# Kernel tuning notes

Measured on AMD Instinct MI355X. Metric: run time of the kernel, lower is better.

The kernel has to match this reference:

```python
import jax, jax.numpy as jnp
from jax import lax
import numpy as np

T, K, KEND = 2048, 4, 8
D, H, WD = 100, 256, 300
V, DICT, C = 20000, 700000, 18


def _build_end_indexed(starts, lens, ids, valid):
    # Group gazetteer words by their END position (the step at which the
    # lattice char cell consumes the word memory cell), padded to KEND slots.
    e_ids = np.zeros((T, KEND), np.int32)
    e_start = np.zeros((T, KEND), np.int32)
    e_mask = np.zeros((T, KEND), np.int32)
    cnt = np.zeros(T, np.int64)
    for t in range(T):
        for k in range(K):
            if valid[t, k]:
                e = int(starts[t, k] + lens[t, k] - 1)
                if cnt[e] < KEND:
                    e_ids[e, cnt[e]] = ids[t, k]
                    e_start[e, cnt[e]] = starts[t, k]
                    e_mask[e, cnt[e]] = 1
                    cnt[e] += 1
    return jnp.asarray(e_ids), jnp.asarray(e_start), jnp.asarray(e_mask)


def setup_inputs():
    ks = jax.random.split(jax.random.key(0), 24)
    inputs = jax.random.randint(ks[0], (1, T), 0, V, dtype=jnp.int32)
    rng = np.random.default_rng(0)
    lens = rng.integers(0, 8, size=(T, K))          # word length; valid iff >= 2
    ids = rng.integers(1, DICT, size=(T, K))        # gazetteer word ids
    pos = np.broadcast_to(np.arange(T)[:, None], (T, K))
    # forward direction: word starts at t, ends at t+len-1
    valid_f = (lens >= 2) & (pos + lens - 1 < T)
    fw_ids, fw_start, fw_mask = _build_end_indexed(pos, lens, ids, valid_f)
    # backward direction, expressed in the flipped frame: start' = T-1-(t+len-1)
    starts_b = T - 1 - (pos + lens - 1)
    valid_b = (lens >= 2) & (starts_b >= 0)
    bw_ids, bw_start, bw_mask = _build_end_indexed(starts_b, lens, ids, valid_b)
    s = 0.08
    nrm = lambda k, shape: jax.random.normal(k, shape, jnp.float32) * s
    p = {}
    i = 1
    for pre in ("fw", "bw"):
        p[pre + "_W_ih"] = nrm(ks[i], (D, 3 * H)); i += 1
        p[pre + "_W_hh"] = nrm(ks[i], (H, 3 * H)); i += 1
        p[pre + "_b"] = jnp.zeros((3 * H,), jnp.float32)
        p[pre + "_aW_ih"] = nrm(ks[i], (D, H)); i += 1
        p[pre + "_aW_hh"] = nrm(ks[i], (H, H)); i += 1
        p[pre + "_ab"] = jnp.zeros((H,), jnp.float32)
        p[pre + "_wW_ih"] = nrm(ks[i], (WD, 3 * H)); i += 1
        p[pre + "_wW_hh"] = nrm(ks[i], (H, 3 * H)); i += 1
        p[pre + "_wb"] = jnp.zeros((3 * H,), jnp.float32)
    out = dict(inputs=inputs, fw_ids=fw_ids, fw_start=fw_start, fw_mask=fw_mask,
               bw_ids=bw_ids, bw_start=bw_start, bw_mask=bw_mask, length=T,
               E=nrm(ks[20], (V, D)), word_table=nrm(ks[21], (DICT, WD)),
               W_lin=nrm(ks[22], (2 * H, C)), b_lin=jnp.zeros((C,), jnp.float32))
    out.update(p)
    return out


def _lattice_pass(x, wemb, start, mask, W_ih, W_hh, b, aW_ih, aW_hh, ab, wW_ih, wW_hh, wb):
    # x: [T,D]; wemb: [T,KEND,WD]; start/mask: [T,KEND]
    Tn, Hn = x.shape[0], W_hh.shape[0]

    def step(carry, xs):
        h, c, Hh, Ch = carry                        # Hh/Ch: [T,H] history of char states
        t, xt, we_t, st, m = xs
        mf = m.astype(x.dtype)[:, None]             # [KEND,1]
        hs, cs = Hh[st], Ch[st]                     # char state at each word's start pos
        # WordLSTMCell: c^w = sigmoid(f)*c_start + sigmoid(i)*tanh(g)
        wi, wf, wg = jnp.split(we_t @ wW_ih + hs @ wW_hh + wb, 3, axis=-1)
        cw = jax.nn.sigmoid(wf) * cs + jax.nn.sigmoid(wi) * jnp.tanh(wg)
        # MultiInputLSTMCell char gates
        ii, oo, gg = jnp.split(xt @ W_ih + h @ W_hh + b, 3, axis=-1)
        i_s, o_s, g_t = jax.nn.sigmoid(ii), jax.nn.sigmoid(oo), jnp.tanh(gg)
        # extra input gate per word, then exp-normalization over {i, alphas}
        alpha = jax.nn.sigmoid(xt @ aW_ih + cw @ aW_hh + ab)   # [KEND,H]
        e_i = jnp.exp(i_s)                                      # [H]
        e_a = jnp.exp(alpha) * mf                               # masked slots drop out
        c_merge = (e_i * g_t + (e_a * cw).sum(0)) / (e_i + e_a.sum(0))
        c_plain = (1.0 - i_s) * c + i_s * g_t                   # no-word branch (f = 1-i)
        c_new = jnp.where(jnp.any(m > 0), c_merge, c_plain)
        h_new = o_s * jnp.tanh(c_new)
        return (h_new, c_new, Hh.at[t].set(h_new), Ch.at[t].set(c_new)), h_new

    z = lambda *sh: jnp.zeros(sh, x.dtype)
    init = (z(Hn), z(Hn), z(Tn, Hn), z(Tn, Hn))
    _, hseq = lax.scan(step, init, (jnp.arange(Tn), x, wemb, start, mask))
    return hseq                                      # [T,H]


def reference(inputs, fw_ids, fw_start, fw_mask, bw_ids, bw_start, bw_mask, length, E,
              word_table, W_lin, b_lin,
              fw_W_ih, fw_W_hh, fw_b, fw_aW_ih, fw_aW_hh, fw_ab, fw_wW_ih, fw_wW_hh, fw_wb,
              bw_W_ih, bw_W_hh, bw_b, bw_aW_ih, bw_aW_hh, bw_ab, bw_wW_ih, bw_wW_hh, bw_wb):
    x = E[inputs[0]]                                 # [T,D] char embeddings (batch=1)
    hf = _lattice_pass(x, word_table[fw_ids], fw_start, fw_mask,
                       fw_W_ih, fw_W_hh, fw_b, fw_aW_ih, fw_aW_hh, fw_ab,
                       fw_wW_ih, fw_wW_hh, fw_wb)
    hb = _lattice_pass(x[::-1], word_table[bw_ids], bw_start, bw_mask,
                       bw_W_ih, bw_W_hh, bw_b, bw_aW_ih, bw_aW_hh, bw_ab,
                       bw_wW_ih, bw_wW_hh, bw_wb)[::-1]
    return (jnp.concatenate([hf, hb], axis=-1) @ W_lin + b_lin)[None]  # [1,T,C]
```

## Files before the change

### kernel.cpp

```cpp
#include <hip/hip_runtime.h>
#include <hip/hip_bf16.h>


#define TSEQ 2048
#define KEND 8
#define DEMB 100
#define H    256
#define H3   768
#define WD   300
#define CCLS 18
#define NTH  256

typedef __attribute__((ext_vector_type(8))) short bf16x8;
typedef __attribute__((ext_vector_type(4))) float f32x4;

#define LO_AT  0
#define LO_A1  131072
#define LO_VS  131584
#define LO_UR  133120
#define LO_RC  143872
#define LO_A2  152064
#define LO_AWS 156288
#define LO_MT  160384
#define SMEM_SCAN 160640

__device__ __forceinline__ float sigf(float x) { return 1.0f / (1.0f + expf(-x)); }
__device__ __forceinline__ float bf2f(unsigned u) { return __uint_as_float(u << 16); }
__device__ __forceinline__ unsigned f2bf(float f) {
  union { float f; unsigned u; } x; x.f = f;
  unsigned r = x.u + 0x7fffu + ((x.u >> 16) & 1u);
  return r >> 16;
}

__global__ __launch_bounds__(64) void k_pack(
    const float* __restrict__ W_hh_f, const float* __restrict__ wW_hh_f, const float* __restrict__ aW_hh_f,
    const float* __restrict__ W_hh_b, const float* __restrict__ wW_hh_b, const float* __restrict__ aW_hh_b,
    unsigned short* __restrict__ Wpk)
{
  const int T = blockIdx.x, dir = blockIdx.y;
  const int lane = threadIdx.x;
  const float* Wg = dir ? W_hh_b  : W_hh_f;
  const float* Ww = dir ? wW_hh_b : wW_hh_f;
  const float* Wa = dir ? aW_hh_b : aW_hh_f;
  for (int ks = 0; ks < 8; ++ks) {
    bf16x8 sv;
#pragma unroll
    for (int e = 0; e < 8; ++e) {
      const int k = ks * 32 + (lane >> 4) * 8 + e;
      float f;
      if (T < 96) {
        const int c = T * 16 + (lane & 15);
        f = (c < H3) ? Wg[(size_t)k * H3 + c] : Ww[(size_t)k * H3 + (c - H3)];
      } else {
        const int c = (T - 96) * 16 + (lane & 15);
        f = Wa[(size_t)k * H + c];
      }
      sv[e] = (short)f2bf(f);
    }
    *(bf16x8*)(Wpk + (((size_t)dir * 112 + T) * 8 + ks) * 512 + lane * 8) = sv;
  }
}

__global__ __launch_bounds__(256) void k_embed(
    const int* __restrict__ inputs, const float* __restrict__ E,
    const float* __restrict__ W_ih_f, const float* __restrict__ b_f,
    const float* __restrict__ aW_ih_f, const float* __restrict__ ab_f,
    const float* __restrict__ W_ih_b, const float* __restrict__ b_b,
    const float* __restrict__ aW_ih_b, const float* __restrict__ ab_b,
    __hip_bfloat16* __restrict__ xg, float* __restrict__ xa)
{
  const int t = blockIdx.x, dir = blockIdx.y;
  const int tid = threadIdx.x;
  const float* W_ih = dir ? W_ih_b : W_ih_f;
  const float* bb   = dir ? b_b    : b_f;
  const float* aW   = dir ? aW_ih_b : aW_ih_f;
  const float* ab   = dir ? ab_b   : ab_f;
  const int src = dir ? (TSEQ - 1 - t) : t;

  __shared__ float xr[DEMB];
  if (tid < DEMB) xr[tid] = E[(size_t)inputs[src] * DEMB + tid];
  __syncthreads();

  float a0 = bb[tid], a1 = bb[H + tid], a2 = bb[2 * H + tid], a3 = ab[tid];
  for (int r = 0; r < DEMB; r += 4) {
    const float4 e4 = *reinterpret_cast<const float4*>(&xr[r]);
    const float ev[4] = {e4.x, e4.y, e4.z, e4.w};
#pragma unroll
    for (int kk = 0; kk < 4; ++kk) {
      const float* wp = W_ih + (size_t)(r + kk) * H3 + tid;
      a0 += ev[kk] * wp[0];
      a1 += ev[kk] * wp[H];
      a2 += ev[kk] * wp[2 * H];
      a3 += ev[kk] * aW[(size_t)(r + kk) * H + tid];
    }
  }
  __hip_bfloat16* xgrow = xg + ((size_t)dir * TSEQ + t) * H3;
  xgrow[tid]         = __float2bfloat16(a0);
  xgrow[H + tid]     = __float2bfloat16(a1);
  xgrow[2 * H + tid] = __float2bfloat16(a2);
  xa[((size_t)dir * TSEQ + t) * H + tid] = a3;
}

__global__ __launch_bounds__(256) void k_wordgates(
    const int* __restrict__ fw_ids, const int* __restrict__ fw_mask,
    const int* __restrict__ bw_ids, const int* __restrict__ bw_mask,
    const float* __restrict__ word_table,
    const float* __restrict__ wW_ih_f, const float* __restrict__ wb_f,
    const float* __restrict__ wW_ih_b, const float* __restrict__ wb_b,
    __hip_bfloat16* __restrict__ wg)
{
  const int t = blockIdx.x, dir = blockIdx.y;
  const int tid = threadIdx.x;
  const int* ids = (dir ? bw_ids : fw_ids) + t * KEND;
  const int* msk = (dir ? bw_mask : fw_mask) + t * KEND;
  const float* wW = dir ? wW_ih_b : wW_ih_f;
  const float* wb = dir ? wb_b    : wb_f;

  __shared__ float we[KEND][WD];
  for (int w = 0; w < KEND; ++w) {
    if (msk[w]) {
      const float* src = word_table + (size_t)ids[w] * WD;
      for (int i = tid; i < WD; i += 256) we[w][i] = src[i];
    }
  }
  __syncthreads();

  __hip_bfloat16* out = wg + ((size_t)dir * TSEQ + t) * KEND * H3;
  for (int w = 0; w < KEND; ++w) {
    if (!msk[w]) continue;
    float a0 = wb[tid], a1 = wb[H + tid], a2 = wb[2 * H + tid];
    for (int r = 0; r < WD; r += 4) {
      const float4 e4 = *reinterpret_cast<const float4*>(&we[w][r]);
      const float ev[4] = {e4.x, e4.y, e4.z, e4.w};
#pragma unroll
      for (int kk = 0; kk < 4; ++kk) {
        const float* wp = wW + (size_t)(r + kk) * H3 + tid;
        a0 += ev[kk] * wp[0];
        a1 += ev[kk] * wp[H];
        a2 += ev[kk] * wp[2 * H];
      }
    }
    out[w * H3 + tid]         = __float2bfloat16(a0);
    out[w * H3 + H + tid]     = __float2bfloat16(a1);
    out[w * H3 + 2 * H + tid] = __float2bfloat16(a2);
  }
}

__global__ __launch_bounds__(NTH, 1) void k_scan(
    const __hip_bfloat16* __restrict__ xg, const float* __restrict__ xa,
    const __hip_bfloat16* __restrict__ wgG, float* __restrict__ hseq,
    const int* __restrict__ fw_start, const int* __restrict__ fw_mask,
    const int* __restrict__ bw_start, const int* __restrict__ bw_mask,
    const unsigned short* __restrict__ Wpk,
    unsigned long long* __restrict__ xb, unsigned* __restrict__ xf)
{
  const int gid = blockIdx.x;
  if (gid != 0 && gid != 1 && gid != 8 && gid != 9) return;
  const int dir  = gid & 1;
  const int side = gid >> 3;

  extern __shared__ char smem[];
  unsigned short* A1_16 = (unsigned short*)(smem + LO_A1);
  unsigned short* vS16  = (unsigned short*)(smem + LO_VS);
  unsigned short* ur16  = (unsigned short*)(smem + LO_UR);
  float* ringC = (float*)(smem + LO_RC);
  unsigned short* awS16 = (unsigned short*)(smem + LO_AWS);
  int* metaI = (int*)(smem + LO_MT);

  const int tid  = threadIdx.x;
  const int lane = tid & 63;
  const int wv   = tid >> 6;
  const int lmod = lane & 15;
  const int lgrp = lane >> 4;

  const int* startA = dir ? bw_start : fw_start;
  const int* maskA  = dir ? bw_mask  : fw_mask;
  const char* WpkD = (const char*)(Wpk + (size_t)dir * 112 * 8 * 512);

  unsigned long long* myPay = xb + (size_t)((dir * 2 + side) * 2) * 192;
  const unsigned long long* peerPay = xb + (size_t)((dir * 2 + (side ^ 1)) * 2) * 192;
  unsigned* myFlag   = xf + (dir * 2 + side) * 32;
  unsigned* peerFlag = xf + (dir * 2 + (side ^ 1)) * 32;

  bf16x8 rW[12][8];
  {
    const char* rp = WpkD + (size_t)(side * 48 + wv * 12) * 8192 + lane * 16;
#pragma unroll
    for (int n = 0; n < 12; ++n)
#pragma unroll
      for (int ks = 0; ks < 8; ++ks)
        rW[n][ks] = *(const bf16x8*)(rp + (n * 8 + ks) * 1024);
  }
  for (int o = tid * 16; o < 131072; o += NTH * 16)
    *(uint4*)(smem + LO_AT + o) = *(const uint4*)(WpkD + (size_t)96 * 8192 + o);
  if (tid < 32) *(uint4*)(smem + LO_A1 + tid * 16) = uint4{0, 0, 0, 0};
  for (int o = tid * 16; o < 4224; o += NTH * 16)
    *(uint4*)(smem + LO_A2 + o) = uint4{0, 0, 0, 0};
  for (int o = tid * 16; o < 8192; o += NTH * 16)
    *(uint4*)(smem + LO_RC + o) = uint4{0, 0, 0, 0};

  unsigned nxI = 0, nxO = 0, nxG = 0; float nxA = 0.f;
  unsigned cxI = 0, cxO = 0, cxG = 0; float cxA = 0.f;
  int nmt = 0;
  {
    const unsigned short* xr = (const unsigned short*)(xg + (size_t)dir * TSEQ * H3);
    nxI = xr[tid]; nxO = xr[H + tid]; nxG = xr[2 * H + tid];
    nxA = xa[(size_t)dir * TSEQ * H + tid];
    if (wv == 3) {
      if (lane < 8) nmt = maskA[lane];
      else if (lane < 16) nmt = startA[lane - 8];
    }
  }
  __syncthreads();
  if (wv == 3) {
    int mAll[8], sAll[8];
#pragma unroll
    for (int s = 0; s < 8; ++s) { mAll[s] = __shfl(nmt, s); sAll[s] = __shfl(nmt, 8 + s); }
    if (lane == 0) {
      int n = 0;
      for (int s = 0; s < 8; ++s)
        if (mAll[s]) { metaI[1 + n] = s; metaI[9 + n] = sAll[s]; ++n; }
      metaI[0] = n;
    }
  }
  cxI = nxI; cxO = nxO; cxG = nxG; cxA = nxA;
  __syncthreads();

  for (int t = 0; t < TSEQ; ++t) {
    const int par = t & 1;
    const int* mp = metaI + par * 32;
    const int nw = mp[0];
    const int us7 = (t + 6) % 7;
    unsigned short* stage16 = side ? (ur16 + us7 * 768) : vS16;
    unsigned short* rcv16   = side ? vS16 : (ur16 + us7 * 768);

    unsigned short wgv[24];
#pragma unroll
    for (int it = 0; it < 8; ++it) {
      const int u0 = tid + it * NTH;
      if (u0 < nw * 256) {
        const int w = u0 >> 8, j = u0 & 255;
        const int slot = mp[1 + w];
        const unsigned short* wgp =
            (const unsigned short*)wgG + ((size_t)(dir * TSEQ + t) * KEND + slot) * H3 + j;
        wgv[it * 3 + 0] = wgp[0];
        wgv[it * 3 + 1] = wgp[256];
        wgv[it * 3 + 2] = wgp[512];
      }
    }

#pragma unroll
    for (int g = 0; g < 2; ++g) {
      f32x4 acc[6];
#pragma unroll
      for (int n = 0; n < 6; ++n) acc[n] = f32x4{0.f, 0.f, 0.f, 0.f};
#pragma unroll
      for (int ks = 0; ks < 8; ++ks) {
        const bf16x8 av = *(const bf16x8*)(smem + LO_A1 + ks * 64 + lgrp * 16);
#pragma unroll
        for (int n = 0; n < 6; ++n)
          acc[n] = __builtin_amdgcn_mfma_f32_16x16x32_bf16(av, rW[g * 6 + n][ks], acc[n], 0, 0, 0);
      }
      if (lane < 16) {
#pragma unroll
        for (int n = 0; n < 6; ++n)
          stage16[(wv * 12 + g * 6 + n) * 16 + lane] = (unsigned short)f2bf(acc[n][0]);
      }
    }
    __syncthreads();

    if (tid < 192) {
      const unsigned long long q = *(const unsigned long long*)((const char*)stage16 + tid * 8);
      __hip_atomic_store(myPay + par * 192 + tid, q, __ATOMIC_RELAXED, __HIP_MEMORY_SCOPE_AGENT);
    }
    {
      const int tn = (t + 1 < TSEQ) ? t + 1 : TSEQ - 1;
      const unsigned short* xr = (const unsigned short*)(xg + ((size_t)dir * TSEQ + tn) * H3);
      nxI = xr[tid]; nxO = xr[H + tid]; nxG = xr[2 * H + tid];
      nxA = xa[((size_t)dir * TSEQ + tn) * H + tid];
      if (wv == 3) {
        if (lane < 8) nmt = maskA[tn * KEND + lane];
        else if (lane < 16) nmt = startA[tn * KEND + (lane - 8)];
      }
    }
#pragma unroll
    for (int it = 0; it < 8; ++it) {
      const int u0 = tid + it * NTH;
      if (u0 < nw * 256) {
        const int w = u0 >> 8, j = u0 & 255;
        const int s = mp[9 + w];
        if (side == 1 || s != t - 1) {
          const unsigned short* ur = ur16 + (s % 7) * 768;
          const float wi  = bf2f(wgv[it * 3 + 0]) + bf2f(ur[j]);
          const float wf  = bf2f(wgv[it * 3 + 1]) + bf2f(ur[256 + j]);
          const float wgg = bf2f(wgv[it * 3 + 2]) + bf2f(ur[512 + j]);
          const float cs  = ringC[(s & 7) * 256 + j];
          const float cv  = sigf(wf) * cs + sigf(wi) * tanhf(wgg);
          *(unsigned short*)(smem + LO_A2 + w * 528 + j * 2) = (unsigned short)f2bf(cv);
        }
      }
    }
    __syncthreads();

    if (tid == 0) {
      __hip_atomic_store(myFlag, (unsigned)(t + 1), __ATOMIC_RELAXED, __HIP_MEMORY_SCOPE_AGENT);
      while (__hip_atomic_load(peerFlag, __ATOMIC_RELAXED, __HIP_MEMORY_SCOPE_AGENT) < (unsigned)(t + 1))
        __builtin_amdgcn_s_sleep(1);
    }
    __syncthreads();

    if (tid < 192) {
      const unsigned long long q =
          __hip_atomic_load(peerPay + par * 192 + tid, __ATOMIC_RELAXED, __HIP_MEMORY_SCOPE_AGENT);
      *(unsigned long long*)((char*)rcv16 + tid * 8) = q;
    }
    __syncthreads();

    if (side == 0) {
#pragma unroll
      for (int it = 0; it < 8; ++it) {
        const int u0 = tid + it * NTH;
        if (u0 < nw * 256) {
          const int w = u0 >> 8, j = u0 & 255;
          const int s = mp[9 + w];
          if (s == t - 1) {
            const unsigned short* ur = ur16 + (s % 7) * 768;
            const float wi  = bf2f(wgv[it * 3 + 0]) + bf2f(ur[j]);
            const float wf  = bf2f(wgv[it * 3 + 1]) + bf2f(ur[256 + j]);
            const float wgg = bf2f(wgv[it * 3 + 2]) + bf2f(ur[512 + j]);
            const float cs  = ringC[(s & 7) * 256 + j];
            const float cv  = sigf(wf) * cs + sigf(wi) * tanhf(wgg);
            *(unsigned short*)(smem + LO_A2 + w * 528 + j * 2) = (unsigned short)f2bf(cv);
          }
        }
      }
    }
    __syncthreads();

    if (nw > 0) {
      const int r2 = (lmod > 7) ? 7 : lmod;
      f32x4 ac[4];
#pragma unroll
      for (int m = 0; m < 4; ++m) ac[m] = f32x4{0.f, 0.f, 0.f, 0.f};
#pragma unroll
      for (int ks = 0; ks < 8; ++ks) {
        const bf16x8 a2v = *(const bf16x8*)(smem + LO_A2 + r2 * 528 + ks * 64 + lgrp * 16);
#pragma unroll
        for (int m = 0; m < 4; ++m) {
          const bf16x8 b = *(const bf16x8*)(smem + LO_AT + (size_t)(wv * 4 + m) * 8192 + ks * 1024 + lane * 16);
          ac[m] = __builtin_amdgcn_mfma_f32_16x16x32_bf16(a2v, b, ac[m], 0, 0, 0);
        }
      }
#pragma unroll
      for (int m = 0; m < 4; ++m) {
#pragma unroll
        for (int r = 0; r < 4; ++r) {
          const int row = lgrp * 4 + r;
          if (row < nw) awS16[row * 256 + (wv * 4 + m) * 16 + lmod] = (unsigned short)f2bf(ac[m][r]);
        }
      }
    }
    __syncthreads();

    {
      const int j = tid;
      const float i_s = sigf(bf2f(cxI) + bf2f(vS16[j]));
      const float o_s = sigf(bf2f(cxO) + bf2f(vS16[256 + j]));
      const float g_t = tanhf(bf2f(cxG) + bf2f(vS16[512 + j]));
      float cnew;
      if (nw > 0) {
        const float e_i = expf(i_s);
        float num = e_i * g_t, den = e_i;
        for (int w = 0; w < nw; ++w) {
          const float a  = sigf(cxA + bf2f(awS16[w * 256 + j]));
          const float ea = expf(a);
          num += ea * bf2f(*(const unsigned short*)(smem + LO_A2 + w * 528 + j * 2));
          den += ea;
        }
        cnew = num / den;
      } else {
        cnew = (1.f - i_s) * ringC[((t - 1) & 7) * 256 + j] + i_s * g_t;
      }
      const float hnew = o_s * tanhf(cnew);
      ringC[(t & 7) * 256 + j] = cnew;
      A1_16[j] = (unsigned short)f2bf(hnew);
      if (side == 0) hseq[((size_t)dir * TSEQ + t) * H + j] = hnew;
    }
    if (wv == 3) {
      int mAll[8], sAll[8];
#pragma unroll
      for (int s = 0; s < 8; ++s) { mAll[s] = __shfl(nmt, s); sAll[s] = __shfl(nmt, 8 + s); }
      if (lane == 0) {
        int* mq = metaI + ((t + 1) & 1) * 32;
        int n = 0;
        for (int s = 0; s < 8; ++s)
          if (mAll[s]) { mq[1 + n] = s; mq[9 + n] = sAll[s]; ++n; }
        mq[0] = n;
      }
    }
    cxI = nxI; cxO = nxO; cxG = nxG; cxA = nxA;
    __syncthreads();
  }
}

__global__ __launch_bounds__(64) void k_proj(
    const float* __restrict__ hseq, const float* __restrict__ W_lin,
    const float* __restrict__ b_lin, float* __restrict__ out)
{
  const int t = blockIdx.x;
  const int tid = threadIdx.x;
  __shared__ float hrow[2 * H];
  for (int i = tid; i < H; i += 64) {
    hrow[i]     = hseq[(size_t)t * H + i];
    hrow[H + i] = hseq[((size_t)TSEQ + (TSEQ - 1 - t)) * H + i];
  }
  __syncthreads();
  if (tid < CCLS) {
    float acc = b_lin[tid];
    for (int j = 0; j < 2 * H; ++j) acc += hrow[j] * W_lin[(size_t)j * CCLS + tid];
    out[(size_t)t * CCLS + tid] = acc;
  }
}

extern "C" void kernel_launch(void* const* d_in, const int* in_sizes, int n_in,
                              void* d_out, int out_size, void* d_ws, size_t ws_size,
                              hipStream_t stream)
{
  const int* inputs   = (const int*)d_in[0];
  const int* fw_ids   = (const int*)d_in[1];
  const int* fw_start = (const int*)d_in[2];
  const int* fw_mask  = (const int*)d_in[3];
  const int* bw_ids   = (const int*)d_in[4];
  const int* bw_start = (const int*)d_in[5];
  const int* bw_mask  = (const int*)d_in[6];
  const float* E          = (const float*)d_in[8];
  const float* word_table = (const float*)d_in[9];
  const float* W_lin      = (const float*)d_in[10];
  const float* b_lin      = (const float*)d_in[11];
  const float* fw_W_ih  = (const float*)d_in[12];
  const float* fw_W_hh  = (const float*)d_in[13];
  const float* fw_b     = (const float*)d_in[14];
  const float* fw_aW_ih = (const float*)d_in[15];
  const float* fw_aW_hh = (const float*)d_in[16];
  const float* fw_ab    = (const float*)d_in[17];
  const float* fw_wW_ih = (const float*)d_in[18];
  const float* fw_wW_hh = (const float*)d_in[19];
  const float* fw_wb    = (const float*)d_in[20];
  const float* bw_W_ih  = (const float*)d_in[21];
  const float* bw_W_hh  = (const float*)d_in[22];
  const float* bw_b     = (const float*)d_in[23];
  const float* bw_aW_ih = (const float*)d_in[24];
  const float* bw_aW_hh = (const float*)d_in[25];
  const float* bw_ab    = (const float*)d_in[26];
  const float* bw_wW_ih = (const float*)d_in[27];
  const float* bw_wW_hh = (const float*)d_in[28];
  const float* bw_wb    = (const float*)d_in[29];

  char* p = (char*)d_ws;
  __hip_bfloat16* xg = (__hip_bfloat16*)p;  p += (size_t)2 * TSEQ * H3 * 2;
  float* xa   = (float*)p;                  p += (size_t)2 * TSEQ * H * 4;
  float* hseq = (float*)p;                  p += (size_t)2 * TSEQ * H * 4;
  __hip_bfloat16* wg = (__hip_bfloat16*)p;  p += (size_t)2 * TSEQ * KEND * H3 * 2;
  unsigned short* Wpk = (unsigned short*)p; p += (size_t)2 * 112 * 8 * 512 * 2;
  unsigned long long* xb = (unsigned long long*)p; p += (size_t)2 * 2 * 2 * 192 * 8;
  unsigned* xf = (unsigned*)p;              p += 512;

  hipFuncSetAttribute((const void*)k_scan,
                      hipFuncAttributeMaxDynamicSharedMemorySize, SMEM_SCAN);
  hipMemsetAsync(xf, 0, 512, stream);

  k_pack<<<dim3(112, 2), 64, 0, stream>>>(
      fw_W_hh, fw_wW_hh, fw_aW_hh, bw_W_hh, bw_wW_hh, bw_aW_hh, Wpk);
  k_embed<<<dim3(TSEQ, 2), 256, 0, stream>>>(
      inputs, E, fw_W_ih, fw_b, fw_aW_ih, fw_ab, bw_W_ih, bw_b, bw_aW_ih, bw_ab, xg, xa);
  k_wordgates<<<dim3(TSEQ, 2), 256, 0, stream>>>(
      fw_ids, fw_mask, bw_ids, bw_mask, word_table, fw_wW_ih, fw_wb, bw_wW_ih, bw_wb, wg);
  k_scan<<<16, NTH, SMEM_SCAN, stream>>>(
      xg, xa, wg, hseq, fw_start, fw_mask, bw_start, bw_mask, Wpk, xb, xf);
  k_proj<<<TSEQ, 64, 0, stream>>>(hseq, W_lin, b_lin, (float*)d_out);
}
```

Baseline: 14.37 ms.

## Overlap word-cell attention MFMA with peer handshake and skip redundant passes

Signal the step flag right after publishing the payload, then compute the attention-gate MFMA for words whose cell does not depend on the previous step while waiting for the peer block. A second MFMA pass and its barriers run only when some word starts at t-1. The spin-wait drops its sleep, and the hseq write is split between the two sides. This aims to hide cross-block sync latency and remove barriers from steps without late words. The cost is a duplicated MFMA pass on steps that have such words and a busier spin loop.

After: 16.80 ms. +16.9%, slower.

```diff
diff --git a/kernel.cpp b/kernel.cpp
--- a/kernel.cpp
+++ b/kernel.cpp
@@ -233,6 +233,8 @@
     const int us7 = (t + 6) % 7;
     unsigned short* stage16 = side ? (ur16 + us7 * 768) : vS16;
     unsigned short* rcv16   = side ? vS16 : (ur16 + us7 * 768);
+    int hasL2w = 0;
+    for (int w = 0; w < nw; ++w) hasL2w |= (mp[9 + w] == t - 1);
 
     unsigned short wgv[24];
 #pragma unroll
@@ -273,6 +275,11 @@
       const unsigned long long q = *(const unsigned long long*)((const char*)stage16 + tid * 8);
       __hip_atomic_store(myPay + par * 192 + tid, q, __ATOMIC_RELAXED, __HIP_MEMORY_SCOPE_AGENT);
     }
+    __syncthreads();
+
+    if (tid == 0)
+      __hip_atomic_store(myFlag, (unsigned)(t + 1), __ATOMIC_RELAXED, __HIP_MEMORY_SCOPE_AGENT);
+
     {
       const int tn = (t + 1 < TSEQ) ? t + 1 : TSEQ - 1;
       const unsigned short* xr = (const unsigned short*)(xg + ((size_t)dir * TSEQ + tn) * H3);
@@ -300,12 +307,37 @@
         }
       }
     }
-    __syncthreads();
+    if (nw > 0) {
+      __syncthreads();
+
+      {
+        const int r2 = (lmod > 7) ? 7 : lmod;
+        f32x4 ac[4];
+#pragma unroll
+        for (int m = 0; m < 4; ++m) ac[m] = f32x4{0.f, 0.f, 0.f, 0.f};
+#pragma unroll
+        for (int ks = 0; ks < 8; ++ks) {
+          const bf16x8 a2v = *(const bf16x8*)(smem + LO_A2 + r2 * 528 + ks * 64 + lgrp * 16);
+#pragma unroll
+          for (int m = 0; m < 4; ++m) {
+            const bf16x8 b = *(const bf16x8*)(smem + LO_AT + (size_t)(wv * 4 + m) * 8192 + ks * 1024 + lane * 16);
+            ac[m] = __builtin_amdgcn_mfma_f32_16x16x32_bf16(a2v, b, ac[m], 0, 0, 0);
+          }
+        }
+#pragma unroll
+        for (int m = 0; m < 4; ++m) {
+#pragma unroll
+          for (int r = 0; r < 4; ++r) {
+            const int row = lgrp * 4 + r;
+            if (row < nw && mp[9 + row] != t - 1)
+              awS16[row * 256 + (wv * 4 + m) * 16 + lmod] = (unsigned short)f2bf(ac[m][r]);
+          }
+        }
+      }
+    }
 
     if (tid == 0) {
-      __hip_atomic_store(myFlag, (unsigned)(t + 1), __ATOMIC_RELAXED, __HIP_MEMORY_SCOPE_AGENT);
-      while (__hip_atomic_load(peerFlag, __ATOMIC_RELAXED, __HIP_MEMORY_SCOPE_AGENT) < (unsigned)(t + 1))
-        __builtin_amdgcn_s_sleep(1);
+      while (__hip_atomic_load(peerFlag, __ATOMIC_RELAXED, __HIP_MEMORY_SCOPE_AGENT) < (unsigned)(t + 1)) {}
     }
     __syncthreads();
 
@@ -316,51 +348,54 @@
     }
     __syncthreads();
 
-    if (side == 0) {
-#pragma unroll
-      for (int it = 0; it < 8; ++it) {
-        const int u0 = tid + it * NTH;
-        if (u0 < nw * 256) {
-          const int w = u0 >> 8, j = u0 & 255;
-          const int s = mp[9 + w];
-          if (s == t - 1) {
-            const unsigned short* ur = ur16 + (s % 7) * 768;
-            const float wi  = bf2f(wgv[it * 3 + 0]) + bf2f(ur[j]);
-            const float wf  = bf2f(wgv[it * 3 + 1]) + bf2f(ur[256 + j]);
-            const float wgg = bf2f(wgv[it * 3 + 2]) + bf2f(ur[512 + j]);
-            const float cs  = ringC[(s & 7) * 256 + j];
-            const float cv  = sigf(wf) * cs + sigf(wi) * tanhf(wgg);
-            *(unsigned short*)(smem + LO_A2 + w * 528 + j * 2) = (unsigned short)f2bf(cv);
+    if (hasL2w) {
+      if (side == 0) {
+#pragma unroll
+        for (int it = 0; it < 8; ++it) {
+          const int u0 = tid + it * NTH;
+          if (u0 < nw * 256) {
+            const int w = u0 >> 8, j = u0 & 255;
+            const int s = mp[9 + w];
+            if (s == t - 1) {
+              const unsigned short* ur = ur16 + (s % 7) * 768;
+              const float wi  = bf2f(wgv[it * 3 + 0]) + bf2f(ur[j]);
+              const float wf  = bf2f(wgv[it * 3 + 1]) + bf2f(ur[256 + j]);
+              const float wgg = bf2f(wgv[it * 3 + 2]) + bf2f(ur[512 + j]);
+              const float cs  = ringC[(s & 7) * 256 + j];
+              const float cv  = sigf(wf) * cs + sigf(wi) * tanhf(wgg);
+              *(unsigned short*)(smem + LO_A2 + w * 528 + j * 2) = (unsigned short)f2bf(cv);
+            }
           }
         }
       }
-    }
-    __syncthreads();
-
-    if (nw > 0) {
-      const int r2 = (lmod > 7) ? 7 : lmod;
-      f32x4 ac[4];
-#pragma unroll
-      for (int m = 0; m < 4; ++m) ac[m] = f32x4{0.f, 0.f, 0.f, 0.f};
-#pragma unroll
-      for (int ks = 0; ks < 8; ++ks) {
-        const bf16x8 a2v = *(const bf16x8*)(smem + LO_A2 + r2 * 528 + ks * 64 + lgrp * 16);
+      __syncthreads();
+
+      {
+        const int r2 = (lmod > 7) ? 7 : lmod;
+        f32x4 ac[4];
+#pragma unroll
+        for (int m = 0; m < 4; ++m) ac[m] = f32x4{0.f, 0.f, 0.f, 0.f};
+#pragma unroll
+        for (int ks = 0; ks < 8; ++ks) {
+          const bf16x8 a2v = *(const bf16x8*)(smem + LO_A2 + r2 * 528 + ks * 64 + lgrp * 16);
+#pragma unroll
+          for (int m = 0; m < 4; ++m) {
+            const bf16x8 b = *(const bf16x8*)(smem + LO_AT + (size_t)(wv * 4 + m) * 8192 + ks * 1024 + lane * 16);
+            ac[m] = __builtin_amdgcn_mfma_f32_16x16x32_bf16(a2v, b, ac[m], 0, 0, 0);
+          }
+        }
 #pragma unroll
         for (int m = 0; m < 4; ++m) {
-          const bf16x8 b = *(const bf16x8*)(smem + LO_AT + (size_t)(wv * 4 + m) * 8192 + ks * 1024 + lane * 16);
-          ac[m] = __builtin_amdgcn_mfma_f32_16x16x32_bf16(a2v, b, ac[m], 0, 0, 0);
-        }
-      }
-#pragma unroll
-      for (int m = 0; m < 4; ++m) {
-#pragma unroll
-        for (int r = 0; r < 4; ++r) {
-          const int row = lgrp * 4 + r;
-          if (row < nw) awS16[row * 256 + (wv * 4 + m) * 16 + lmod] = (unsigned short)f2bf(ac[m][r]);
-        }
-      }
-    }
-    __syncthreads();
+#pragma unroll
+          for (int r = 0; r < 4; ++r) {
+            const int row = lgrp * 4 + r;
+            if (row < nw && mp[9 + row] == t - 1)
+              awS16[row * 256 + (wv * 4 + m) * 16 + lmod] = (unsigned short)f2bf(ac[m][r]);
+          }
+        }
+      }
+      __syncthreads();
+    }
 
     {
       const int j = tid;
@@ -384,7 +419,8 @@
       const float hnew = o_s * tanhf(cnew);
       ringC[(t & 7) * 256 + j] = cnew;
       A1_16[j] = (unsigned short)f2bf(hnew);
-      if (side == 0) hseq[((size_t)dir * TSEQ + t) * H + j] = hnew;
+      if ((side == 0) == (j < 128))
+        hseq[((size_t)dir * TSEQ + t) * H + j] = hnew;
     }
     if (wv == 3) {
       int mAll[8], sAll[8];
```

## Merge two-block split scan into one block per direction, streaming word weights

Applied to the files above, without the earlier changes.

Replaces the two cooperating blocks per direction, which exchanged half-results through global memory with flag spin-waits every step, with a single block per direction. That block computes both the char-cell gates (register-resident weights) and the word-cell hidden projection, streaming the latter's weights from global or L2 each step in double-buffered register batches. It also skips the word-cell phase and its barriers when no words end at the step, and stores gate pre-activations in fp32. This removes the cross-block handshake latency but doubles the per-step matmul work on one CU and adds global weight reloads every timestep.

New measurement: 34.80 ms. 142% more time.

```diff
diff --git a/kernel.cpp b/kernel.cpp
--- a/kernel.cpp
+++ b/kernel.cpp
@@ -16,13 +16,13 @@
 
 #define LO_AT  0
 #define LO_A1  131072
-#define LO_VS  131584
-#define LO_UR  133120
-#define LO_RC  143872
-#define LO_A2  152064
-#define LO_AWS 156288
-#define LO_MT  160384
-#define SMEM_SCAN 160640
+#define LO_UR  131584
+#define LO_RC  142336
+#define LO_PRE 150528
+#define LO_A2  153600
+#define LO_AWS 157824
+#define LO_MT  161920
+#define SMEM_SCAN 162176
 
 __device__ __forceinline__ float sigf(float x) { return 1.0f / (1.0f + expf(-x)); }
 __device__ __forceinline__ float bf2f(unsigned u) { return __uint_as_float(u << 16); }
@@ -151,19 +151,15 @@
     const __hip_bfloat16* __restrict__ wgG, float* __restrict__ hseq,
     const int* __restrict__ fw_start, const int* __restrict__ fw_mask,
     const int* __restrict__ bw_start, const int* __restrict__ bw_mask,
-    const unsigned short* __restrict__ Wpk,
-    unsigned long long* __restrict__ xb, unsigned* __restrict__ xf)
-{
-  const int gid = blockIdx.x;
-  if (gid != 0 && gid != 1 && gid != 8 && gid != 9) return;
-  const int dir  = gid & 1;
-  const int side = gid >> 3;
+    const unsigned short* __restrict__ Wpk)
+{
+  const int dir = blockIdx.x;
 
   extern __shared__ char smem[];
   unsigned short* A1_16 = (unsigned short*)(smem + LO_A1);
-  unsigned short* vS16  = (unsigned short*)(smem + LO_VS);
   unsigned short* ur16  = (unsigned short*)(smem + LO_UR);
   float* ringC = (float*)(smem + LO_RC);
+  float* preS  = (float*)(smem + LO_PRE);
   unsigned short* awS16 = (unsigned short*)(smem + LO_AWS);
   int* metaI = (int*)(smem + LO_MT);
 
@@ -177,14 +173,9 @@
   const int* maskA  = dir ? bw_mask  : fw_mask;
   const char* WpkD = (const char*)(Wpk + (size_t)dir * 112 * 8 * 512);
 
-  unsigned long long* myPay = xb + (size_t)((dir * 2 + side) * 2) * 192;
-  const unsigned long long* peerPay = xb + (size_t)((dir * 2 + (side ^ 1)) * 2) * 192;
-  unsigned* myFlag   = xf + (dir * 2 + side) * 32;
-  unsigned* peerFlag = xf + (dir * 2 + (side ^ 1)) * 32;
-
   bf16x8 rW[12][8];
   {
-    const char* rp = WpkD + (size_t)(side * 48 + wv * 12) * 8192 + lane * 16;
+    const char* rp = WpkD + (size_t)(wv * 12) * 8192 + lane * 16;
 #pragma unroll
     for (int n = 0; n < 12; ++n)
 #pragma unroll
@@ -226,28 +217,19 @@
   cxI = nxI; cxO = nxO; cxG = nxG; cxA = nxA;
   __syncthreads();
 
+  const char* up = WpkD + (size_t)(48 + 12 * wv) * 8192 + lane * 16;
+
   for (int t = 0; t < TSEQ; ++t) {
     const int par = t & 1;
     const int* mp = metaI + par * 32;
     const int nw = mp[0];
     const int us7 = (t + 6) % 7;
-    unsigned short* stage16 = side ? (ur16 + us7 * 768) : vS16;
-    unsigned short* rcv16   = side ? vS16 : (ur16 + us7 * 768);
-
-    unsigned short wgv[24];
-#pragma unroll
-    for (int it = 0; it < 8; ++it) {
-      const int u0 = tid + it * NTH;
-      if (u0 < nw * 256) {
-        const int w = u0 >> 8, j = u0 & 255;
-        const int slot = mp[1 + w];
-        const unsigned short* wgp =
-            (const unsigned short*)wgG + ((size_t)(dir * TSEQ + t) * KEND + slot) * H3 + j;
-        wgv[it * 3 + 0] = wgp[0];
-        wgv[it * 3 + 1] = wgp[256];
-        wgv[it * 3 + 2] = wgp[512];
-      }
-    }
+
+    bf16x8 bA[8], bB[8];
+#pragma unroll
+    for (int f = 0; f < 8; ++f) bA[f] = *(const bf16x8*)(up + f * 1024);
+#pragma unroll
+    for (int f = 0; f < 8; ++f) bB[f] = *(const bf16x8*)(up + 8192 + f * 1024);
 
 #pragma unroll
     for (int g = 0; g < 2; ++g) {
@@ -264,15 +246,45 @@
       if (lane < 16) {
 #pragma unroll
         for (int n = 0; n < 6; ++n)
-          stage16[(wv * 12 + g * 6 + n) * 16 + lane] = (unsigned short)f2bf(acc[n][0]);
-      }
-    }
-    __syncthreads();
-
-    if (tid < 192) {
-      const unsigned long long q = *(const unsigned long long*)((const char*)stage16 + tid * 8);
-      __hip_atomic_store(myPay + par * 192 + tid, q, __ATOMIC_RELAXED, __HIP_MEMORY_SCOPE_AGENT);
-    }
+          preS[(wv * 12 + g * 6 + n) * 16 + lane] = acc[n][0];
+      }
+    }
+
+    {
+      unsigned short* urow = ur16 + us7 * 768;
+#pragma unroll
+      for (int k = 0; k < 6; ++k) {
+        {
+          f32x4 acc = {0.f, 0.f, 0.f, 0.f};
+#pragma unroll
+          for (int ks = 0; ks < 8; ++ks) {
+            const bf16x8 av = *(const bf16x8*)(smem + LO_A1 + ks * 64 + lgrp * 16);
+            acc = __builtin_amdgcn_mfma_f32_16x16x32_bf16(av, bA[ks], acc, 0, 0, 0);
+          }
+          if (k < 5) {
+#pragma unroll
+            for (int f = 0; f < 8; ++f)
+              bA[f] = *(const bf16x8*)(up + (size_t)(2 * k + 2) * 8192 + f * 1024);
+          }
+          if (lane < 16) urow[(wv * 12 + 2 * k) * 16 + lane] = (unsigned short)f2bf(acc[0]);
+        }
+        {
+          f32x4 acc = {0.f, 0.f, 0.f, 0.f};
+#pragma unroll
+          for (int ks = 0; ks < 8; ++ks) {
+            const bf16x8 av = *(const bf16x8*)(smem + LO_A1 + ks * 64 + lgrp * 16);
+            acc = __builtin_amdgcn_mfma_f32_16x16x32_bf16(av, bB[ks], acc, 0, 0, 0);
+          }
+          if (k < 5) {
+#pragma unroll
+            for (int f = 0; f < 8; ++f)
+              bB[f] = *(const bf16x8*)(up + (size_t)(2 * k + 3) * 8192 + f * 1024);
+          }
+          if (lane < 16) urow[(wv * 12 + 2 * k + 1) * 16 + lane] = (unsigned short)f2bf(acc[0]);
+        }
+      }
+    }
+
     {
       const int tn = (t + 1 < TSEQ) ? t + 1 : TSEQ - 1;
       const unsigned short* xr = (const unsigned short*)(xg + ((size_t)dir * TSEQ + tn) * H3);
@@ -283,90 +295,60 @@
         else if (lane < 16) nmt = startA[tn * KEND + (lane - 8)];
       }
     }
-#pragma unroll
-    for (int it = 0; it < 8; ++it) {
-      const int u0 = tid + it * NTH;
-      if (u0 < nw * 256) {
-        const int w = u0 >> 8, j = u0 & 255;
-        const int s = mp[9 + w];
-        if (side == 1 || s != t - 1) {
-          const unsigned short* ur = ur16 + (s % 7) * 768;
-          const float wi  = bf2f(wgv[it * 3 + 0]) + bf2f(ur[j]);
-          const float wf  = bf2f(wgv[it * 3 + 1]) + bf2f(ur[256 + j]);
-          const float wgg = bf2f(wgv[it * 3 + 2]) + bf2f(ur[512 + j]);
-          const float cs  = ringC[(s & 7) * 256 + j];
-          const float cv  = sigf(wf) * cs + sigf(wi) * tanhf(wgg);
-          *(unsigned short*)(smem + LO_A2 + w * 528 + j * 2) = (unsigned short)f2bf(cv);
-        }
-      }
-    }
     __syncthreads();
 
-    if (tid == 0) {
-      __hip_atomic_store(myFlag, (unsigned)(t + 1), __ATOMIC_RELAXED, __HIP_MEMORY_SCOPE_AGENT);
-      while (__hip_atomic_load(peerFlag, __ATOMIC_RELAXED, __HIP_MEMORY_SCOPE_AGENT) < (unsigned)(t + 1))
-        __builtin_amdgcn_s_sleep(1);
-    }
-    __syncthreads();
-
-    if (tid < 192) {
-      const unsigned long long q =
-          __hip_atomic_load(peerPay + par * 192 + tid, __ATOMIC_RELAXED, __HIP_MEMORY_SCOPE_AGENT);
-      *(unsigned long long*)((char*)rcv16 + tid * 8) = q;
-    }
-    __syncthreads();
-
-    if (side == 0) {
+    if (nw > 0) {
 #pragma unroll
       for (int it = 0; it < 8; ++it) {
         const int u0 = tid + it * NTH;
         if (u0 < nw * 256) {
           const int w = u0 >> 8, j = u0 & 255;
           const int s = mp[9 + w];
-          if (s == t - 1) {
-            const unsigned short* ur = ur16 + (s % 7) * 768;
-            const float wi  = bf2f(wgv[it * 3 + 0]) + bf2f(ur[j]);
-            const float wf  = bf2f(wgv[it * 3 + 1]) + bf2f(ur[256 + j]);
-            const float wgg = bf2f(wgv[it * 3 + 2]) + bf2f(ur[512 + j]);
-            const float cs  = ringC[(s & 7) * 256 + j];
-            const float cv  = sigf(wf) * cs + sigf(wi) * tanhf(wgg);
-            *(unsigned short*)(smem + LO_A2 + w * 528 + j * 2) = (unsigned short)f2bf(cv);
-          }
-        }
-      }
-    }
-    __syncthreads();
-
-    if (nw > 0) {
-      const int r2 = (lmod > 7) ? 7 : lmod;
-      f32x4 ac[4];
-#pragma unroll
-      for (int m = 0; m < 4; ++m) ac[m] = f32x4{0.f, 0.f, 0.f, 0.f};
-#pragma unroll
-      for (int ks = 0; ks < 8; ++ks) {
-        const bf16x8 a2v = *(const bf16x8*)(smem + LO_A2 + r2 * 528 + ks * 64 + lgrp * 16);
+          const int slot = mp[1 + w];
+          const unsigned short* wgp =
+              (const unsigned short*)wgG + ((size_t)(dir * TSEQ + t) * KEND + slot) * H3 + j;
+          const unsigned short* ur = ur16 + (s % 7) * 768;
+          const float wi  = bf2f(wgp[0])   + bf2f(ur[j]);
+          const float wf  = bf2f(wgp[256]) + bf2f(ur[256 + j]);
+          const float wgg = bf2f(wgp[512]) + bf2f(ur[512 + j]);
+          const float cs  = ringC[(s & 7) * 256 + j];
+          const float cv  = sigf(wf) * cs + sigf(wi) * tanhf(wgg);
+          *(unsigned short*)(smem + LO_A2 + w * 528 + j * 2) = (unsigned short)f2bf(cv);
+        }
+      }
+      __syncthreads();
+
+      {
+        const int r2 = (lmod > 7) ? 7 : lmod;
+        f32x4 ac[4];
+#pragma unroll
+        for (int m = 0; m < 4; ++m) ac[m] = f32x4{0.f, 0.f, 0.f, 0.f};
+#pragma unroll
+        for (int ks = 0; ks < 8; ++ks) {
+          const bf16x8 a2v = *(const bf16x8*)(smem + LO_A2 + r2 * 528 + ks * 64 + lgrp * 16);
+#pragma unroll
+          for (int m = 0; m < 4; ++m) {
+            const bf16x8 b = *(const bf16x8*)(smem + LO_AT + (size_t)(wv * 4 + m) * 8192 + ks * 1024 + lane * 16);
+            ac[m] = __builtin_amdgcn_mfma_f32_16x16x32_bf16(a2v, b, ac[m], 0, 0, 0);
+          }
+        }
 #pragma unroll
         for (int m = 0; m < 4; ++m) {
-          const bf16x8 b = *(const bf16x8*)(smem + LO_AT + (size_t)(wv * 4 + m) * 8192 + ks * 1024 + lane * 16);
-          ac[m] = __builtin_amdgcn_mfma_f32_16x16x32_bf16(a2v, b, ac[m], 0, 0, 0);
-        }
-      }
-#pragma unroll
-      for (int m = 0; m < 4; ++m) {
-#pragma unroll
-        for (int r = 0; r < 4; ++r) {
-          const int row = lgrp * 4 + r;
-          if (row < nw) awS16[row * 256 + (wv * 4 + m) * 16 + lmod] = (unsigned short)f2bf(ac[m][r]);
-        }
-      }
-    }
-    __syncthreads();
+#pragma unroll
+          for (int r = 0; r < 4; ++r) {
+            const int row = lgrp * 4 + r;
+            if (row < nw) awS16[row * 256 + (wv * 4 + m) * 16 + lmod] = (unsigned short)f2bf(ac[m][r]);
+          }
+        }
+      }
+      __syncthreads();
+    }
 
     {
       const int j = tid;
-      const float i_s = sigf(bf2f(cxI) + bf2f(vS16[j]));
-      const float o_s = sigf(bf2f(cxO) + bf2f(vS16[256 + j]));
-      const float g_t = tanhf(bf2f(cxG) + bf2f(vS16[512 + j]));
+      const float i_s = sigf(bf2f(cxI) + preS[j]);
+      const float o_s = sigf(bf2f(cxO) + preS[256 + j]);
+      const float g_t = tanhf(bf2f(cxG) + preS[512 + j]);
       float cnew;
       if (nw > 0) {
         const float e_i = expf(i_s);
@@ -384,7 +366,7 @@
       const float hnew = o_s * tanhf(cnew);
       ringC[(t & 7) * 256 + j] = cnew;
       A1_16[j] = (unsigned short)f2bf(hnew);
-      if (side == 0) hseq[((size_t)dir * TSEQ + t) * H + j] = hnew;
+      hseq[((size_t)dir * TSEQ + t) * H + j] = hnew;
     }
     if (wv == 3) {
       int mAll[8], sAll[8];
@@ -462,12 +444,9 @@
   float* hseq = (float*)p;                  p += (size_t)2 * TSEQ * H * 4;
   __hip_bfloat16* wg = (__hip_bfloat16*)p;  p += (size_t)2 * TSEQ * KEND * H3 * 2;
   unsigned short* Wpk = (unsigned short*)p; p += (size_t)2 * 112 * 8 * 512 * 2;
-  unsigned long long* xb = (unsigned long long*)p; p += (size_t)2 * 2 * 2 * 192 * 8;
-  unsigned* xf = (unsigned*)p;              p += 512;
 
   hipFuncSetAttribute((const void*)k_scan,
                       hipFuncAttributeMaxDynamicSharedMemorySize, SMEM_SCAN);
-  hipMemsetAsync(xf, 0, 512, stream);
 
   k_pack<<<dim3(112, 2), 64, 0, stream>>>(
       fw_W_hh, fw_wW_hh, fw_aW_hh, bw_W_hh, bw_wW_hh, bw_aW_hh, Wpk);
@@ -475,7 +454,7 @@
       inputs, E, fw_W_ih, fw_b, fw_aW_ih, fw_ab, bw_W_ih, bw_b, bw_aW_ih, bw_ab, xg, xa);
   k_wordgates<<<dim3(TSEQ, 2), 256, 0, stream>>>(
       fw_ids, fw_mask, bw_ids, bw_mask, word_table, fw_wW_ih, fw_wb, bw_wW_ih, bw_wb, wg);
-  k_scan<<<16, NTH, SMEM_SCAN, stream>>>(
-      xg, xa, wg, hseq, fw_start, fw_mask, bw_start, bw_mask, Wpk, xb, xf);
+  k_scan<<<2, NTH, SMEM_SCAN, stream>>>(
+      xg, xa, wg, hseq, fw_start, fw_mask, bw_start, bw_mask, Wpk);
   k_proj<<<TSEQ, 64, 0, stream>>>(hseq, W_lin, b_lin, (float*)d_out);
 }
```
